# Optimization experiments

Measured on AMD Instinct MI355X. Metric: run time of the kernel, lower is better.

The kernel has to match this reference:

```python
import jax, jax.numpy as jnp
import numpy as np

NORM_EPS = 1e-6
QK_SCALE = 1.0 / 128.0  # 1/d_head (muP)
ROTARY_BASE = 10000
INFTY_APPROX = 1e30

B, T, M, H, D = 2, 2048, 1024, 8, 128


def _rmsnorm(x, eps=NORM_EPS):
    # normalize over the last (head) dim; no learned gains (norm_gains=False)
    ms = jnp.mean(jnp.square(x), axis=-1, keepdims=True)
    return x / jnp.sqrt(ms + eps)


def _rope(x, base=ROTARY_BASE):
    # x: [b, h, t, d]; rotate (even-half, odd-half) pairs as in the source
    length, width = x.shape[-2], x.shape[-1]
    half = width // 2
    pos = jnp.arange(length, dtype=x.dtype)[:, None]            # [t, 1]
    freqs = jnp.power(jnp.asarray(base, x.dtype), -jnp.arange(half, dtype=x.dtype) / half)[None, :]
    rad = pos * freqs                                            # [t, half]
    cos = jnp.cos(rad)[None, None]
    sin = jnp.sin(rad)[None, None]
    even, odd = jnp.split(x, 2, axis=-1)
    return jnp.concatenate([even * cos - odd * sin, even * sin + odd * cos], axis=-1)


def setup_inputs() -> dict:
    key = jax.random.key(0)
    ks = jax.random.split(key, 5)
    std = M ** -0.5
    return {
        "x": jax.random.normal(ks[0], (B, T, M), jnp.float32),
        "wq": jax.random.normal(ks[1], (M, H, D), jnp.float32) * std,
        "wk": jax.random.normal(ks[2], (M, H, D), jnp.float32) * std,
        "wv": jax.random.normal(ks[3], (M, H, D), jnp.float32) * std,
        "wo": jax.random.normal(ks[4], (H, D, M), jnp.float32) * std,
    }


def reference(x, wq, wk, wv, wo):
    # projections: [b, h, t, d]
    q = jnp.einsum('bim,mhd->bhid', x, wq)
    k = jnp.einsum('bim,mhd->bhid', x, wk)
    v = jnp.einsum('bim,mhd->bhid', x, wv)
    # qk RMSNorm (norm_gains=False)
    q = _rmsnorm(q)
    k = _rmsnorm(k)
    # inline RoPE
    q = _rope(q)
    k = _rope(k)
    # scaled scores: mult applied to both q and k (mult^2 = qk_scale)
    mult = jnp.asarray(QK_SCALE ** 0.5, q.dtype)
    s = jnp.einsum('bhid,bhjd->bhij', q * mult, k * mult)
    # causal mask: subtract large constant where i < j
    t = s.shape[-1]
    mask = (jnp.arange(t)[:, None] < jnp.arange(t)[None, :]).astype(s.dtype)
    s = s - jnp.asarray(INFTY_APPROX, s.dtype) * mask[None, None]
    p = jax.nn.softmax(s, axis=-1)
    o = jnp.einsum('bhij,bhjd->bhid', p, v)
    return jnp.einsum('bhid,hdm->bim', o, wo)
```

## Files before the change

kernel.cpp:

```cpp
#include <hip/hip_runtime.h>
#include <hip/hip_bf16.h>
#include <math.h>

#define B_  2
#define T_  2048
#define M_  1024
#define H_  8
#define D_  128
#define NROW (B_ * T_)
#define HD  (H_ * D_)

#define NORM_EPS 1e-6f
#define QK_MULT  0.08838834764831845f
#define LN_BASE_64 0.14391156510f

typedef short bf16x8  __attribute__((ext_vector_type(8)));
typedef float f32x4   __attribute__((ext_vector_type(4)));
typedef float f32x16  __attribute__((ext_vector_type(16)));

static __device__ __forceinline__ unsigned short f2bf(float f) {
    union { __hip_bfloat16 h; unsigned short u; } cv;
    cv.h = __float2bfloat16(f);
    return cv.u;
}
static __device__ __forceinline__ float bf2f(unsigned short u) {
    union { unsigned short u; __hip_bfloat16 h; } cv;
    cv.u = u;
    return __bfloat162float(cv.h);
}
static __device__ __forceinline__ unsigned int pk2bf(float a, float b) {
    return ((unsigned int)f2bf(b) << 16) | f2bf(a);
}

static __device__ __forceinline__ void gload_lds16(const unsigned short* g,
                                                   unsigned short* l) {
    __builtin_amdgcn_global_load_lds(
        (const __attribute__((address_space(1))) void*)g,
        (__attribute__((address_space(3))) void*)l, 16, 0, 0);
}

__global__ __launch_bounds__(256) void prep(const float* __restrict__ x,
                                            const float* __restrict__ w0,
                                            const float* __restrict__ w1,
                                            const float* __restrict__ w2,
                                            const float* __restrict__ w3,
                                            unsigned short* __restrict__ xb,
                                            unsigned short* __restrict__ wqkvT,
                                            unsigned short* __restrict__ woT)
{
    __shared__ float t[32][33];
    const int z = blockIdx.z;
    if (z == 4) {
        const size_t base = ((size_t)blockIdx.y * 32 + blockIdx.x) * 4096;
        #pragma unroll
        for (int it = 0; it < 4; ++it) {
            const size_t i = base + it * 1024 + threadIdx.x * 4;
            const float4 v = *(const float4*)(x + i);
            ushort4 o;
            o.x = f2bf(v.x); o.y = f2bf(v.y); o.z = f2bf(v.z); o.w = f2bf(v.w);
            *(ushort4*)(xb + i) = o;
        }
        return;
    }
    const float* in = z == 0 ? w0 : (z == 1 ? w1 : (z == 2 ? w2 : w3));
    unsigned short* out = z < 3 ? (wqkvT + (size_t)z * 1024 * 1024) : woT;

    const int tx = threadIdx.x & 31;
    const int ty = threadIdx.x >> 5;
    const int n0 = blockIdx.x * 32;
    const int k0 = blockIdx.y * 32;
    #pragma unroll
    for (int r = 0; r < 4; ++r)
        t[ty + r * 8][tx] = in[(size_t)(k0 + ty + r * 8) * 1024 + n0 + tx];
    __syncthreads();
    #pragma unroll
    for (int r = 0; r < 4; ++r)
        out[(size_t)(n0 + ty + r * 8) * 1024 + k0 + tx] = f2bf(t[tx][ty + r * 8]);
}

__global__ __launch_bounds__(256) void gemm_qkv(const unsigned short* __restrict__ A,
                                                const unsigned short* __restrict__ Bt,
                                                unsigned short* __restrict__ oq,
                                                unsigned short* __restrict__ ok,
                                                unsigned short* __restrict__ vt)
{
    __shared__ unsigned short As[128 * 64];
    __shared__ unsigned short Bs[128 * 64];

    const int tid  = threadIdx.x;
    const int lane = tid & 63;
    const int w    = tid >> 6;
    const int g    = lane >> 4;
    const int lc   = lane & 15;

    const int m0 = blockIdx.y * 128;
    const int n0 = blockIdx.x * 128;

    const unsigned short* aBase = A  + (size_t)m0 * 1024;
    const unsigned short* bBase = Bt + (size_t)n0 * 1024;

    f32x4 acc[2][8];
    #pragma unroll
    for (int i = 0; i < 2; ++i)
        #pragma unroll
        for (int j = 0; j < 8; ++j)
            acc[i][j] = (f32x4){0.f, 0.f, 0.f, 0.f};

    for (int kt = 0; kt < 16; ++kt) {
        const int k0 = kt * 64;
        #pragma unroll
        for (int it = 0; it < 4; ++it) {
            const int u  = tid + it * 256;
            const int r2 = u >> 3;
            const int s2 = u & 7;
            const int sg = s2 ^ (r2 & 7);
            gload_lds16(aBase + (size_t)r2 * 1024 + k0 + sg * 8, &As[u * 8]);
            gload_lds16(bBase + (size_t)r2 * 1024 + k0 + sg * 8, &Bs[u * 8]);
        }
        __syncthreads();

        #pragma unroll
        for (int dc = 0; dc < 2; ++dc) {
            const int sw = ((dc * 4 + g) ^ (lc & 7)) << 3;
            bf16x8 af[2], bfr[8];
            #pragma unroll
            for (int i = 0; i < 2; ++i)
                af[i] = *(const bf16x8*)&As[(w * 32 + i * 16 + lc) * 64 + sw];
            #pragma unroll
            for (int j = 0; j < 8; ++j)
                bfr[j] = *(const bf16x8*)&Bs[(j * 16 + lc) * 64 + sw];

            #pragma unroll
            for (int i = 0; i < 2; ++i)
                #pragma unroll
                for (int j = 0; j < 8; ++j)
                    acc[i][j] = __builtin_amdgcn_mfma_f32_16x16x32_bf16(af[i], bfr[j], acc[i][j], 0, 0, 0);
        }
        __syncthreads();
    }

    const int which = n0 >> 10;
    const int ncol0 = n0 & 1023;
    if (which < 2) {
        unsigned short* outp = which == 0 ? oq : ok;
        float freq[4];
        #pragma unroll
        for (int j = 0; j < 4; ++j)
            freq[j] = __expf(-(float)(j * 16 + lc) * LN_BASE_64);

        #pragma unroll
        for (int i = 0; i < 2; ++i)
            #pragma unroll
            for (int r = 0; r < 4; ++r) {
                float s = 0.f;
                #pragma unroll
                for (int j = 0; j < 8; ++j) s += acc[i][j][r] * acc[i][j][r];
                #pragma unroll
                for (int off = 1; off < 16; off <<= 1) s += __shfl_xor(s, off);
                const float rms = rsqrtf(s * (1.0f / 128.0f) + NORM_EPS) * QK_MULT;

                const int trow = m0 + w * 32 + i * 16 + g * 4 + r;
                const float tpos = (float)(trow & (T_ - 1));
                unsigned short* op = outp + (size_t)trow * 1024 + ncol0;
                #pragma unroll
                for (int j = 0; j < 4; ++j) {
                    float sn, cs;
                    __sincosf(tpos * freq[j], &sn, &cs);
                    const float e = acc[i][j][r] * rms;
                    const float o = acc[i][j + 4][r] * rms;
                    op[j * 16 + lc]      = f2bf(e * cs - o * sn);
                    op[j * 16 + lc + 64] = f2bf(e * sn + o * cs);
                }
            }
    } else {
        const int b2 = m0 >> 11;
        const int hh = ncol0 >> 7;
        #pragma unroll
        for (int i = 0; i < 2; ++i) {
            const int t = (m0 & 2047) + w * 32 + i * 16 + g * 4;
            #pragma unroll
            for (int j = 0; j < 8; ++j) {
                const int dd = j * 16 + lc;
                uint2 val;
                val.x = pk2bf(acc[i][j][0], acc[i][j][1]);
                val.y = pk2bf(acc[i][j][2], acc[i][j][3]);
                *(uint2*)(vt + (((size_t)(b2 * 8 + hh) * 128 + dd) * T_ + t)) = val;
            }
        }
    }
}

__global__ __launch_bounds__(256) void gemm_out(const unsigned short* __restrict__ A,
                                                const unsigned short* __restrict__ Bt,
                                                float* __restrict__ cf)
{
    __shared__ unsigned short As[128 * 64];
    __shared__ unsigned short Bs[64 * 64];

    const int tid  = threadIdx.x;
    const int lane = tid & 63;
    const int w    = tid >> 6;
    const int g    = lane >> 4;
    const int lc   = lane & 15;
    const int wm   = w >> 1;
    const int wn   = w & 1;

    const int m0 = blockIdx.y * 128;
    const int n0 = blockIdx.x * 64;

    const unsigned short* aBase = A  + (size_t)m0 * 1024;
    const unsigned short* bBase = Bt + (size_t)n0 * 1024;

    f32x4 acc[4][2];
    #pragma unroll
    for (int i = 0; i < 4; ++i)
        #pragma unroll
        for (int j = 0; j < 2; ++j)
            acc[i][j] = (f32x4){0.f, 0.f, 0.f, 0.f};

    for (int kt = 0; kt < 16; ++kt) {
        const int k0 = kt * 64;
        #pragma unroll
        for (int it = 0; it < 4; ++it) {
            const int u  = tid + it * 256;
            const int r2 = u >> 3;
            const int sg = (u & 7) ^ (r2 & 7);
            gload_lds16(aBase + (size_t)r2 * 1024 + k0 + sg * 8, &As[u * 8]);
        }
        #pragma unroll
        for (int it = 0; it < 2; ++it) {
            const int u  = tid + it * 256;
            const int r2 = u >> 3;
            const int sg = (u & 7) ^ (r2 & 7);
            gload_lds16(bBase + (size_t)r2 * 1024 + k0 + sg * 8, &Bs[u * 8]);
        }
        __syncthreads();

        #pragma unroll
        for (int dc = 0; dc < 2; ++dc) {
            const int sw = ((dc * 4 + g) ^ (lc & 7)) << 3;
            bf16x8 af[4], bfr[2];
            #pragma unroll
            for (int i = 0; i < 4; ++i)
                af[i] = *(const bf16x8*)&As[(wm * 64 + i * 16 + lc) * 64 + sw];
            #pragma unroll
            for (int j = 0; j < 2; ++j)
                bfr[j] = *(const bf16x8*)&Bs[(wn * 32 + j * 16 + lc) * 64 + sw];

            #pragma unroll
            for (int i = 0; i < 4; ++i)
                #pragma unroll
                for (int j = 0; j < 2; ++j)
                    acc[i][j] = __builtin_amdgcn_mfma_f32_16x16x32_bf16(af[i], bfr[j], acc[i][j], 0, 0, 0);
        }
        __syncthreads();
    }

    #pragma unroll
    for (int i = 0; i < 4; ++i) {
        const int mrow = m0 + wm * 64 + i * 16 + g * 4;
        #pragma unroll
        for (int j = 0; j < 2; ++j) {
            const int nc = n0 + wn * 32 + j * 16 + lc;
            #pragma unroll
            for (int r = 0; r < 4; ++r)
                cf[(size_t)(mrow + r) * 1024 + nc] = acc[i][j][r];
        }
    }
}

__global__ __launch_bounds__(256) void flash_attn(const unsigned short* __restrict__ qb,
                                                  const unsigned short* __restrict__ kb,
                                                  const unsigned short* __restrict__ vt,
                                                  unsigned short* __restrict__ o)
{
    __shared__ __align__(16) unsigned short smem[2 * 64 * 128 + 2 * 128 * 64 + 128];
    unsigned short* KsB = smem;
    unsigned short* VsB = smem + 2 * 64 * 128;
    float* lscr = (float*)(smem + 2 * 64 * 128 + 2 * 128 * 64);
    float* scr  = (float*)smem;

    const int tid  = threadIdx.x;
    const int lane = tid & 63;
    const int w    = tid >> 6;
    const int wj   = w >> 1;
    const int wq2  = w & 1;
    const int qcol = lane & 31;
    const int hi   = lane >> 5;

    const int bh = blockIdx.x;
    const int h  = bh & (H_ - 1);
    const int b  = bh >> 3;
    const int yy = blockIdx.y;
    const int qt = (yy & 1) ? (31 - (yy >> 1)) : (yy >> 1);
    const int q0 = qt * 64;

    const size_t bhbase  = (size_t)b * T_ * HD + (size_t)h * 128;
    const size_t bhvbase = (size_t)bh * 128 * T_;

    int mI[4];
    size_t srcKoff[4], srcVoff[4];
    #pragma unroll
    for (int it = 0; it < 4; ++it) {
        const int m = (w * 4 + it) * 64 + lane;
        mI[it] = m;
        const int jK = m >> 4, cK = (m & 15) ^ (jK & 15);
        srcKoff[it] = (size_t)jK * 1024 + cK * 8;
        const int dV = m >> 3, cV = (m & 7) ^ (dV & 7);
        srcVoff[it] = (size_t)dV * T_ + cV * 8;
    }
    const unsigned short* kgb = kb + bhbase;
    const unsigned short* vgb = vt + bhvbase;

    bf16x8 qf[8];
    {
        const unsigned short* qp = qb + bhbase + (size_t)(q0 + wq2 * 32 + qcol) * 1024 + hi * 8;
        #pragma unroll
        for (int ks = 0; ks < 8; ++ks)
            qf[ks] = *(const bf16x8*)(qp + ks * 16);
    }

    float lsum = 0.f;
    f32x16 otacc[4];
    #pragma unroll
    for (int dch = 0; dch < 4; ++dch)
        #pragma unroll
        for (int r = 0; r < 16; ++r) otacc[dch][r] = 0.f;

    #pragma unroll
    for (int it = 0; it < 4; ++it) {
        gload_lds16(kgb + srcKoff[it], &KsB[mI[it] * 8]);
        gload_lds16(vgb + srcVoff[it], &VsB[mI[it] * 8]);
    }

    for (int jt = 0; jt <= qt; ++jt) {
        const int cur = jt & 1;
        unsigned short* Ks = KsB + cur * (64 * 128);
        unsigned short* Vs = VsB + cur * (128 * 64);
        __syncthreads();

        if (jt < qt) {
            const size_t j0n = (size_t)(jt + 1) * 64;
            unsigned short* Kn = KsB + (cur ^ 1) * (64 * 128);
            unsigned short* Vn = VsB + (cur ^ 1) * (128 * 64);
            #pragma unroll
            for (int it = 0; it < 4; ++it) {
                gload_lds16(kgb + j0n * 1024 + srcKoff[it], &Kn[mI[it] * 8]);
                gload_lds16(vgb + j0n + srcVoff[it], &Vn[mI[it] * 8]);
            }
        }

        const bool dead = (jt == qt) && (wj > wq2);
        if (!dead) {
            f32x16 sacc;
            #pragma unroll
            for (int r = 0; r < 16; ++r) sacc[r] = 0.f;
            const int jrow = wj * 32 + qcol;
            #pragma unroll
            for (int ks = 0; ks < 8; ++ks) {
                const int c = ks * 2 + hi;
                bf16x8 af = *(const bf16x8*)&Ks[(jrow * 16 + (c ^ (lane & 15))) * 8];
                sacc = __builtin_amdgcn_mfma_f32_32x32x16_bf16(af, qf[ks], sacc, 0, 0, 0);
            }

            if (jt == qt && wj == wq2) {
                #pragma unroll
                for (int r = 0; r < 16; ++r) {
                    const int jl = (r & 3) + 8 * (r >> 2) + 4 * hi;
                    if (qcol < jl) sacc[r] = -1e30f;
                }
            }

            unsigned int dw[8];
            #pragma unroll
            for (int m2 = 0; m2 < 8; ++m2) {
                const float p0 = __expf(sacc[2 * m2]);
                const float p1 = __expf(sacc[2 * m2 + 1]);
                lsum += p0 + p1;
                dw[m2] = pk2bf(p0, p1);
            }
            unsigned int ex[8];
            #pragma unroll
            for (int m2 = 0; m2 < 8; ++m2)
                ex[m2] = (unsigned int)__shfl_xor((int)dw[m2], 32);

            #pragma unroll
            for (int ks2 = 0; ks2 < 2; ++ks2) {
                union { unsigned int u[4]; bf16x8 v; } pf;
                pf.u[0] = hi ? ex[4 * ks2 + 2] : dw[4 * ks2 + 0];
                pf.u[1] = hi ? ex[4 * ks2 + 3] : dw[4 * ks2 + 1];
                pf.u[2] = hi ? dw[4 * ks2 + 2] : ex[4 * ks2 + 0];
                pf.u[3] = hi ? dw[4 * ks2 + 3] : ex[4 * ks2 + 1];
                #pragma unroll
                for (int dch = 0; dch < 4; ++dch) {
                    const int c = wj * 4 + ks2 * 2 + hi;
                    const int drow = dch * 32 + qcol;
                    bf16x8 af = *(const bf16x8*)&Vs[(drow * 8 + (c ^ (lane & 7))) * 8];
                    otacc[dch] = __builtin_amdgcn_mfma_f32_32x32x16_bf16(af, pf.v, otacc[dch], 0, 0, 0);
                }
            }
        }
    }

    lsum += __shfl_xor(lsum, 32);
    __syncthreads();

    if (wj == 1) {
        float* s0 = scr + (size_t)(wq2 * 32 + qcol) * 129;
        #pragma unroll
        for (int dch = 0; dch < 4; ++dch)
            #pragma unroll
            for (int r = 0; r < 16; ++r)
                s0[dch * 32 + (r & 3) + 8 * (r >> 2) + 4 * hi] = otacc[dch][r];
        if (hi == 0) lscr[wq2 * 32 + qcol] = lsum;
    }
    __syncthreads();
    if (wj == 0) {
        const float l = lsum + lscr[wq2 * 32 + qcol];
        const float inv = 1.0f / l;
        const float* s0 = scr + (size_t)(wq2 * 32 + qcol) * 129;
        unsigned short* op = o + bhbase + (size_t)(q0 + wq2 * 32 + qcol) * 1024;
        #pragma unroll
        for (int dch = 0; dch < 4; ++dch) {
            #pragma unroll
            for (int k4 = 0; k4 < 4; ++k4) {
                const int d0 = dch * 32 + 8 * k4 + 4 * hi;
                const float f0 = (otacc[dch][4 * k4 + 0] + s0[d0 + 0]) * inv;
                const float f1 = (otacc[dch][4 * k4 + 1] + s0[d0 + 1]) * inv;
                const float f2 = (otacc[dch][4 * k4 + 2] + s0[d0 + 2]) * inv;
                const float f3 = (otacc[dch][4 * k4 + 3] + s0[d0 + 3]) * inv;
                uint2 val;
                val.x = pk2bf(f0, f1);
                val.y = pk2bf(f2, f3);
                *(uint2*)(op + d0) = val;
            }
        }
    }
}

extern "C" void kernel_launch(void* const* d_in, const int* in_sizes, int n_in,
                              void* d_out, int out_size, void* d_ws, size_t ws_size,
                              hipStream_t stream)
{
    const float* x  = (const float*)d_in[0];
    const float* wq = (const float*)d_in[1];
    const float* wk = (const float*)d_in[2];
    const float* wv = (const float*)d_in[3];
    const float* wo = (const float*)d_in[4];
    float* out = (float*)d_out;

    const size_t SZ = (size_t)NROW * HD;
    unsigned short* qb    = (unsigned short*)d_ws;
    unsigned short* kb    = qb + SZ;
    unsigned short* vt    = kb + SZ;
    unsigned short* ob    = vt + SZ;
    unsigned short* xb    = ob + SZ;
    unsigned short* wqkvT = xb + SZ;
    unsigned short* woT   = wqkvT + 3 * 1024 * 1024;

    prep<<<dim3(32, 32, 5), 256, 0, stream>>>(x, wq, wk, wv, wo, xb, wqkvT, woT);

    gemm_qkv<<<dim3(24, 32), 256, 0, stream>>>(xb, wqkvT, qb, kb, vt);

    flash_attn<<<dim3(B_ * H_, 32), 256, 0, stream>>>(qb, kb, vt, ob);

    gemm_out<<<dim3(16, 32), 256, 0, stream>>>(ob, woT, out);
}
```

Measured before the change: 189.0 us.

## Double-buffer LDS tiles in QKV and output GEMMs to overlap loads with MFMA

Both projection GEMMs now use two LDS buffers. Each iteration prefetches the next K-tile into the other buffer right after the barrier, so global-to-LDS loads overlap the MFMA work on the current tile, and one barrier per iteration is removed. Source and destination offsets are computed once up front. The cost is doubled shared memory per block (64KB for the QKV GEMM), which may lower occupancy.

```diff
diff --git a/kernel.cpp b/kernel.cpp
--- a/kernel.cpp
+++ b/kernel.cpp
@@ -84,8 +84,8 @@
                                                 unsigned short* __restrict__ ok,
                                                 unsigned short* __restrict__ vt)
 {
-    __shared__ unsigned short As[128 * 64];
-    __shared__ unsigned short Bs[128 * 64];
+    __shared__ unsigned short As[2][128 * 64];
+    __shared__ unsigned short Bs[2][128 * 64];
 
     const int tid  = threadIdx.x;
     const int lane = tid & 63;
@@ -99,6 +99,17 @@
     const unsigned short* aBase = A  + (size_t)m0 * 1024;
     const unsigned short* bBase = Bt + (size_t)n0 * 1024;
 
+    int dstOff[4];
+    size_t srcOff[4];
+    #pragma unroll
+    for (int it = 0; it < 4; ++it) {
+        const int u  = tid + it * 256;
+        const int r2 = u >> 3;
+        const int sg = (u & 7) ^ (r2 & 7);
+        dstOff[it] = u * 8;
+        srcOff[it] = (size_t)r2 * 1024 + sg * 8;
+    }
+
     f32x4 acc[2][8];
     #pragma unroll
     for (int i = 0; i < 2; ++i)
@@ -106,18 +117,24 @@
         for (int j = 0; j < 8; ++j)
             acc[i][j] = (f32x4){0.f, 0.f, 0.f, 0.f};
 
+    #pragma unroll
+    for (int it = 0; it < 4; ++it) {
+        gload_lds16(aBase + srcOff[it], &As[0][dstOff[it]]);
+        gload_lds16(bBase + srcOff[it], &Bs[0][dstOff[it]]);
+    }
+
     for (int kt = 0; kt < 16; ++kt) {
-        const int k0 = kt * 64;
-        #pragma unroll
-        for (int it = 0; it < 4; ++it) {
-            const int u  = tid + it * 256;
-            const int r2 = u >> 3;
-            const int s2 = u & 7;
-            const int sg = s2 ^ (r2 & 7);
-            gload_lds16(aBase + (size_t)r2 * 1024 + k0 + sg * 8, &As[u * 8]);
-            gload_lds16(bBase + (size_t)r2 * 1024 + k0 + sg * 8, &Bs[u * 8]);
-        }
+        const int cur = kt & 1;
         __syncthreads();
+
+        if (kt < 15) {
+            const int k0n = (kt + 1) * 64;
+            #pragma unroll
+            for (int it = 0; it < 4; ++it) {
+                gload_lds16(aBase + srcOff[it] + k0n, &As[cur ^ 1][dstOff[it]]);
+                gload_lds16(bBase + srcOff[it] + k0n, &Bs[cur ^ 1][dstOff[it]]);
+            }
+        }
 
         #pragma unroll
         for (int dc = 0; dc < 2; ++dc) {
@@ -125,10 +142,10 @@
             bf16x8 af[2], bfr[8];
             #pragma unroll
             for (int i = 0; i < 2; ++i)
-                af[i] = *(const bf16x8*)&As[(w * 32 + i * 16 + lc) * 64 + sw];
+                af[i] = *(const bf16x8*)&As[cur][(w * 32 + i * 16 + lc) * 64 + sw];
             #pragma unroll
             for (int j = 0; j < 8; ++j)
-                bfr[j] = *(const bf16x8*)&Bs[(j * 16 + lc) * 64 + sw];
+                bfr[j] = *(const bf16x8*)&Bs[cur][(j * 16 + lc) * 64 + sw];
 
             #pragma unroll
             for (int i = 0; i < 2; ++i)
@@ -136,7 +153,6 @@
                 for (int j = 0; j < 8; ++j)
                     acc[i][j] = __builtin_amdgcn_mfma_f32_16x16x32_bf16(af[i], bfr[j], acc[i][j], 0, 0, 0);
         }
-        __syncthreads();
     }
 
     const int which = n0 >> 10;
@@ -194,8 +210,8 @@
                                                 const unsigned short* __restrict__ Bt,
                                                 float* __restrict__ cf)
 {
-    __shared__ unsigned short As[128 * 64];
-    __shared__ unsigned short Bs[64 * 64];
+    __shared__ unsigned short As[2][128 * 64];
+    __shared__ unsigned short Bs[2][64 * 64];
 
     const int tid  = threadIdx.x;
     const int lane = tid & 63;
@@ -211,6 +227,25 @@
     const unsigned short* aBase = A  + (size_t)m0 * 1024;
     const unsigned short* bBase = Bt + (size_t)n0 * 1024;
 
+    int dstA[4], dstB[2];
+    size_t srcA[4], srcB[2];
+    #pragma unroll
+    for (int it = 0; it < 4; ++it) {
+        const int u  = tid + it * 256;
+        const int r2 = u >> 3;
+        const int sg = (u & 7) ^ (r2 & 7);
+        dstA[it] = u * 8;
+        srcA[it] = (size_t)r2 * 1024 + sg * 8;
+    }
+    #pragma unroll
+    for (int it = 0; it < 2; ++it) {
+        const int u  = tid + it * 256;
+        const int r2 = u >> 3;
+        const int sg = (u & 7) ^ (r2 & 7);
+        dstB[it] = u * 8;
+        srcB[it] = (size_t)r2 * 1024 + sg * 8;
+    }
+
     f32x4 acc[4][2];
     #pragma unroll
     for (int i = 0; i < 4; ++i)
@@ -218,23 +253,26 @@
         for (int j = 0; j < 2; ++j)
             acc[i][j] = (f32x4){0.f, 0.f, 0.f, 0.f};
 
+    #pragma unroll
+    for (int it = 0; it < 4; ++it)
+        gload_lds16(aBase + srcA[it], &As[0][dstA[it]]);
+    #pragma unroll
+    for (int it = 0; it < 2; ++it)
+        gload_lds16(bBase + srcB[it], &Bs[0][dstB[it]]);
+
     for (int kt = 0; kt < 16; ++kt) {
-        const int k0 = kt * 64;
-        #pragma unroll
-        for (int it = 0; it < 4; ++it) {
-            const int u  = tid + it * 256;
-            const int r2 = u >> 3;
-            const int sg = (u & 7) ^ (r2 & 7);
-            gload_lds16(aBase + (size_t)r2 * 1024 + k0 + sg * 8, &As[u * 8]);
-        }
-        #pragma unroll
-        for (int it = 0; it < 2; ++it) {
-            const int u  = tid + it * 256;
-            const int r2 = u >> 3;
-            const int sg = (u & 7) ^ (r2 & 7);
-            gload_lds16(bBase + (size_t)r2 * 1024 + k0 + sg * 8, &Bs[u * 8]);
-        }
+        const int cur = kt & 1;
         __syncthreads();
+
+        if (kt < 15) {
+            const int k0n = (kt + 1) * 64;
+            #pragma unroll
+            for (int it = 0; it < 4; ++it)
+                gload_lds16(aBase + srcA[it] + k0n, &As[cur ^ 1][dstA[it]]);
+            #pragma unroll
+            for (int it = 0; it < 2; ++it)
+                gload_lds16(bBase + srcB[it] + k0n, &Bs[cur ^ 1][dstB[it]]);
+        }
 
         #pragma unroll
         for (int dc = 0; dc < 2; ++dc) {
@@ -242,10 +280,10 @@
             bf16x8 af[4], bfr[2];
             #pragma unroll
             for (int i = 0; i < 4; ++i)
-                af[i] = *(const bf16x8*)&As[(wm * 64 + i * 16 + lc) * 64 + sw];
+                af[i] = *(const bf16x8*)&As[cur][(wm * 64 + i * 16 + lc) * 64 + sw];
             #pragma unroll
             for (int j = 0; j < 2; ++j)
-                bfr[j] = *(const bf16x8*)&Bs[(wn * 32 + j * 16 + lc) * 64 + sw];
+                bfr[j] = *(const bf16x8*)&Bs[cur][(wn * 32 + j * 16 + lc) * 64 + sw];
 
             #pragma unroll
             for (int i = 0; i < 4; ++i)
@@ -253,7 +291,6 @@
                 for (int j = 0; j < 2; ++j)
                     acc[i][j] = __builtin_amdgcn_mfma_f32_16x16x32_bf16(af[i], bfr[j], acc[i][j], 0, 0, 0);
         }
-        __syncthreads();
     }
 
     #pragma unroll
```

Result: no change. 186.6 us (-1.3%).
